# Kernel optimization log

Measured on AMD Instinct MI355X. Metric: run time of the kernel, lower is better.

## Reference

```python
import jax, jax.numpy as jnp
import numpy as np

N_E = 8192
E_DIM = 256
BETA = 0.25


def setup_inputs() -> dict:
    key = jax.random.key(0)
    k1, k2 = jax.random.split(key)
    z = jax.random.normal(k1, (16, E_DIM, 32, 32), dtype=jnp.float32)
    # matches torch init: uniform(-1/n_e, 1/n_e)
    emb_w = jax.random.uniform(k2, (N_E, E_DIM), dtype=jnp.float32,
                               minval=-1.0 / N_E, maxval=1.0 / N_E)
    return {"z": z, "emb_w": emb_w}


def reference(z, emb_w):
    B, C, H, W = z.shape
    zt = jnp.transpose(z, (0, 2, 3, 1))          # b h w c
    zf = zt.reshape(-1, C)                        # [N, e_dim]
    # d[n, k] = ||zf_n||^2 + ||e_k||^2 - 2 zf_n . e_k
    d = (jnp.sum(zf * zf, axis=1, keepdims=True)
         + jnp.sum(emb_w * emb_w, axis=1)
         - 2.0 * jnp.einsum('bd,nd->bn', zf, emb_w))
    idx = jnp.argmin(d, axis=1)                   # [N]
    z_q = emb_w[idx].reshape(zt.shape)            # b h w c
    sg = jax.lax.stop_gradient
    # legacy=True loss
    loss = jnp.mean((sg(z_q) - zt) ** 2) + BETA * jnp.mean((z_q - sg(zt)) ** 2)
    # straight-through estimator
    z_q_st = zt + sg(z_q - zt)
    z_q_out = jnp.transpose(z_q_st, (0, 3, 1, 2))  # b c h w
    return z_q_out, loss, idx.reshape(B, H, W)
```

## Files before the change

kernel.cpp:

```cpp
#include <hip/hip_runtime.h>
#include <math.h>

typedef unsigned int uint;
typedef unsigned short ushort;
typedef unsigned long long u64;
typedef __attribute__((ext_vector_type(8))) short short8;
typedef __attribute__((ext_vector_type(4))) float f32x4;

#define WS_ZT   0ull
#define WS_ZPK  16777216ull
#define WS_EPK  25165824ull
#define WS_SUMZ 29360128ull
#define WS_GMAX 29425664ull
#define WS_BEST 62980096ull
#define WS_LOSS 63111168ull

#define DOT_MARGIN 1.5e-4f

__device__ __forceinline__ ushort f2bf(float f) {
  uint b = __float_as_uint(f);
  b += 0x7fffu + ((b >> 16) & 1u);
  return (ushort)(b >> 16);
}
__device__ __forceinline__ uint ford(float f) {
  uint b = __float_as_uint(f);
  return (b & 0x80000000u) ? ~b : (b | 0x80000000u);
}
__device__ __forceinline__ void gload_lds16(const void* g, void* l) {
  __builtin_amdgcn_global_load_lds(
      (const __attribute__((address_space(1))) unsigned int*)g,
      (__attribute__((address_space(3))) unsigned int*)l, 16, 0, 0);
}

__global__ __launch_bounds__(256) void prep_z(const float* __restrict__ z,
                                              float* __restrict__ zt,
                                              ushort* __restrict__ zpk) {
  __shared__ float tile[64][65];
  const int bid = blockIdx.x;
  const int kt = bid & 3, hwt = (bid >> 2) & 15, b = bid >> 6;
  const int t = threadIdx.x, lane = t & 63, grp = t >> 6;
  const float* src = z + b * 262144 + (kt * 64) * 1024 + hwt * 64;
  for (int kk = grp; kk < 64; kk += 4)
    tile[kk][lane] = src[kk * 1024 + lane];
  __syncthreads();
  for (int rr = grp; rr < 64; rr += 4) {
    const int n = b * 1024 + hwt * 64 + rr;
    zt[n * 256 + kt * 64 + lane] = tile[lane][rr];
  }
  for (int u = t; u < 512; u += 256) {
    const int n_loc = u & 63, kg = u >> 6;
    const int n = b * 1024 + hwt * 64 + n_loc;
    const int k0 = kt * 64 + kg * 8;
    short8 s;
#pragma unroll
    for (int j = 0; j < 8; ++j) s[j] = (short)f2bf(tile[kg * 8 + j][n_loc]);
    *(short8*)(zpk + (size_t)(n >> 4) * 4096 + (k0 >> 5) * 512 +
               ((k0 >> 3) & 3) * 128 + (n & 15) * 8) = s;
  }
}

__global__ __launch_bounds__(256) void prep_e(const float* __restrict__ emb,
                                              ushort* __restrict__ epk) {
  const int u = blockIdx.x * 256 + threadIdx.x;
  const int c = u >> 5, k0 = (u & 31) * 8;
  const float4 v0 = *(const float4*)(emb + c * 256 + k0);
  const float4 v1 = *(const float4*)(emb + c * 256 + k0 + 4);
  short8 s;
  s[0] = (short)f2bf(v0.x); s[1] = (short)f2bf(v0.y);
  s[2] = (short)f2bf(v0.z); s[3] = (short)f2bf(v0.w);
  s[4] = (short)f2bf(v1.x); s[5] = (short)f2bf(v1.y);
  s[6] = (short)f2bf(v1.z); s[7] = (short)f2bf(v1.w);
  *(short8*)(epk + (size_t)(c >> 4) * 4096 + (k0 >> 5) * 512 +
             ((k0 >> 3) & 3) * 128 + (c & 15) * 8) = s;
}

__global__ __launch_bounds__(256) void zsum_kernel(const float* __restrict__ z,
                                                   float* __restrict__ sumz) {
  const int n = (blockIdx.x << 8) + threadIdx.x;
  const int b = n >> 10, hw = n & 1023;
  const float* zb = z + b * 262144 + hw;
  float s = 0.f;
#pragma unroll 8
  for (int c = 0; c < 256; ++c) { const float v = zb[c << 10]; s += v * v; }
  sumz[n] = s;
}

__global__ __launch_bounds__(256) void gemm_screen(const ushort* __restrict__ zpk,
                                                   const ushort* __restrict__ epk,
                                                   uint* __restrict__ gmax) {
  __shared__ ushort Cs[16384];
  const int t = threadIdx.x;
  const int w = t >> 6, lane = t & 63;
  const int bid = blockIdx.x;
  const int x = bid & 7, y = bid >> 3;
  const int colb = (y & 15) * 8 + x;
  const int rowg = y >> 4;
  const int n0 = rowg << 10;
  const int m16 = lane & 15, q = lane >> 4;
  const int cix = x * 64 + (y & 15) * 4 + q;

#pragma unroll
  for (int f2 = 0; f2 < 8; ++f2) {
    const int f = w * 8 + f2;
    gload_lds16(epk + (size_t)colb * 16384 + f * 512 + lane * 8, (char*)Cs + f * 1024);
  }

  short8 z0[4], z1[4], z2[4];
  const ushort* zs0 = zpk + ((size_t)(n0 >> 4) + w * 4) * 4096 + lane * 8;
#pragma unroll
  for (int jr = 0; jr < 4; ++jr) z0[jr] = *(const short8*)(zs0 + jr * 4096);
#pragma unroll
  for (int jr = 0; jr < 4; ++jr) z1[jr] = *(const short8*)(zs0 + jr * 4096 + 512);
  __syncthreads();

  for (int strip = 0; strip < 4; ++strip) {
    const int rbase = n0 + strip * 256 + w * 64;
    const ushort* zb = zpk + (size_t)(rbase >> 4) * 4096 + lane * 8;
    const ushort* zbn = (strip < 3) ? (zb + 16 * 4096) : zb;
    f32x4 acc[4][4];
#pragma unroll
    for (int i = 0; i < 4; ++i)
#pragma unroll
      for (int j = 0; j < 4; ++j) acc[i][j] = {0.f, 0.f, 0.f, 0.f};

#pragma unroll
    for (int s32 = 0; s32 < 8; ++s32) {
      const ushort* pf = (s32 < 6) ? (zb + (s32 + 2) * 512) : (zbn + (s32 - 6) * 512);
#pragma unroll
      for (int jr = 0; jr < 4; ++jr) z2[jr] = *(const short8*)(pf + jr * 4096);
      short8 cv[4];
#pragma unroll
      for (int ic = 0; ic < 4; ++ic)
        cv[ic] = *(const short8*)&Cs[(size_t)(ic * 8 + s32) * 512 + lane * 8];
#pragma unroll
      for (int ic = 0; ic < 4; ++ic)
#pragma unroll
        for (int jr = 0; jr < 4; ++jr)
          acc[ic][jr] = __builtin_amdgcn_mfma_f32_16x16x32_bf16(cv[ic], z0[jr],
                                                                acc[ic][jr], 0, 0, 0);
#pragma unroll
      for (int jr = 0; jr < 4; ++jr) { z0[jr] = z1[jr]; z1[jr] = z2[jr]; }
    }

#pragma unroll
    for (int jr = 0; jr < 4; ++jr) {
      uint pk[4];
#pragma unroll
      for (int ic = 0; ic < 4; ++ic) {
        float m = fmaxf(fmaxf(acc[ic][jr][0], acc[ic][jr][1]),
                        fmaxf(acc[ic][jr][2], acc[ic][jr][3]));
        m = fmaxf(m, __shfl_xor(m, 16, 64));
        const float o = __shfl_xor(m, 32, 64);
        const float glo = (q & 2) ? o : m;
        const float ghi = (q & 2) ? m : o;
        pk[ic] = (uint)f2bf(glo) | ((uint)f2bf(ghi) << 16);
      }
      const uint sv = (q == 0) ? pk[0] : (q == 1) ? pk[1] : (q == 2) ? pk[2] : pk[3];
      __builtin_nontemporal_store(sv,
          &gmax[(size_t)(rbase + jr * 16 + m16) * 512 + cix]);
    }
  }
}

__global__ __launch_bounds__(256) void select_rescore(const uint* __restrict__ gmax,
                                                      const float* __restrict__ zt,
                                                      const float* __restrict__ emb,
                                                      const float* __restrict__ sumz,
                                                      u64* __restrict__ best) {
  const int t = threadIdx.x, w = t >> 6, lane = t & 63;
  const int n = (blockIdx.x << 2) + w;
  __shared__ float zrow[4][256];
  __shared__ ushort hits[4][128];
  ((float4*)zrow[w])[lane] = ((const float4*)(zt + (size_t)n * 256))[lane];
  const uint4 r0 = ((const uint4*)(gmax + (size_t)n * 512))[lane];
  const uint4 r1 = ((const uint4*)(gmax + (size_t)n * 512))[lane + 64];
  const uint uv[8] = {r0.x, r0.y, r0.z, r0.w, r1.x, r1.y, r1.z, r1.w};
  float m = -INFINITY;
#pragma unroll
  for (int j = 0; j < 8; ++j) {
    m = fmaxf(m, __uint_as_float(uv[j] << 16));
    m = fmaxf(m, __uint_as_float(uv[j] & 0xffff0000u));
  }
#pragma unroll
  for (int off = 1; off < 64; off <<= 1) m = fmaxf(m, __shfl_xor(m, off, 64));
  const float thr = m - DOT_MARGIN;
  const u64 below = (1ull << lane) - 1ull;
  int base = 0;
#pragma unroll
  for (int j = 0; j < 8; ++j) {
    const int ui = (j < 4) ? lane * 4 + j : 256 + lane * 4 + (j - 4);
    {
      const bool hit = __uint_as_float(uv[j] << 16) >= thr;
      const u64 msk = __ballot(hit);
      if (hit) {
        const int p = base + (int)__popcll(msk & below);
        if (p < 128) hits[w][p] = (ushort)(ui * 2);
      }
      base += (int)__popcll(msk);
    }
    {
      const bool hit = __uint_as_float(uv[j] & 0xffff0000u) >= thr;
      const u64 msk = __ballot(hit);
      if (hit) {
        const int p = base + (int)__popcll(msk & below);
        if (p < 128) hits[w][p] = (ushort)(ui * 2 + 1);
      }
      base += (int)__popcll(msk);
    }
  }
  __threadfence_block();
  int K = base > 128 ? 128 : base;
  const float sz = sumz[n];
  u64 bk = ~0ull;
  for (int id = lane; id < K * 8; id += 64) {
    const int gid = hits[w][id >> 3];
    const int ci = gid >> 1, h = gid & 1;
    const int c = ((ci >> 2) & 15) * 512 + (ci >> 6) * 64 + (ci & 3) * 16 +
                  h * 8 + (id & 7);
    const float4* ea = (const float4*)(emb + c * 256);
    const float4* za = (const float4*)zrow[w];
    float sdot = 0.f, se = 0.f;
#pragma unroll 8
    for (int k = 0; k < 64; ++k) {
      const float4 a = za[k], e = ea[k];
      sdot = fmaf(a.x, e.x, sdot); sdot = fmaf(a.y, e.y, sdot);
      sdot = fmaf(a.z, e.z, sdot); sdot = fmaf(a.w, e.w, sdot);
      se = fmaf(e.x, e.x, se); se = fmaf(e.y, e.y, se);
      se = fmaf(e.z, e.z, se); se = fmaf(e.w, e.w, se);
    }
    const float d = (sz + se) - 2.f * sdot;
    const u64 key = ((u64)ford(d) << 32) | (uint)c;
    if (key < bk) bk = key;
  }
#pragma unroll
  for (int off = 1; off < 64; off <<= 1) {
    const u64 o = (((u64)(uint)__shfl_xor((int)(bk >> 32), off, 64)) << 32) |
                  (uint)__shfl_xor((int)(bk & 0xffffffffu), off, 64);
    if (o < bk) bk = o;
  }
  if (lane == 0) best[n] = bk;
}

__global__ __launch_bounds__(256) void gather_kernel(const float* __restrict__ z,
                                                     const float* __restrict__ emb,
                                                     const u64* __restrict__ best,
                                                     float* __restrict__ out,
                                                     double* __restrict__ loss_acc,
                                                     uint* __restrict__ done) {
  const int t = threadIdx.x;
  const int n0 = blockIdx.x << 6;
  const int n = n0 + (t & 63);
  const int idx = (int)(best[n] & 0xffffffffull);
  const int b_i = n >> 10, hw = n & 1023;
  const int c0 = t >> 6;
  const float* zb = z + b_i * 262144 + hw;
  float* ob = out + b_i * 262144 + hw;
  const float* eb = emb + idx * 256;
  float lsum = 0.f;
#pragma unroll 4
  for (int c = c0; c < 256; c += 4) {
    const float ev = eb[c];
    const float zv = zb[c << 10];
    ob[c << 10] = ev;
    const float d = ev - zv;
    lsum += d * d;
  }
  if (c0 == 0) out[4194305 + n] = (float)idx;
#pragma unroll
  for (int off = 32; off; off >>= 1) lsum += __shfl_down(lsum, off, 64);
  __shared__ double wsum[4];
  if ((t & 63) == 0) wsum[t >> 6] = (double)lsum;
  __syncthreads();
  if (t == 0) {
    atomicAdd(loss_acc, wsum[0] + wsum[1] + wsum[2] + wsum[3]);
    __threadfence();
    if (atomicAdd(done, 1u) == 255u) {
      __threadfence();
      out[4194304] = (float)(1.25 * (*(volatile double*)loss_acc) / 4194304.0);
    }
  }
}

extern "C" void kernel_launch(void* const* d_in, const int* in_sizes, int n_in,
                              void* d_out, int out_size, void* d_ws, size_t ws_size,
                              hipStream_t stream) {
  const float* z = (const float*)d_in[0];
  const float* emb = (const float*)d_in[1];
  float* out = (float*)d_out;
  char* ws = (char*)d_ws;
  float* zt = (float*)(ws + WS_ZT);
  ushort* zpk = (ushort*)(ws + WS_ZPK);
  ushort* epk = (ushort*)(ws + WS_EPK);
  float* sumz = (float*)(ws + WS_SUMZ);
  uint* gmax = (uint*)(ws + WS_GMAX);
  u64* best = (u64*)(ws + WS_BEST);
  double* loss_acc = (double*)(ws + WS_LOSS);
  uint* done = (uint*)(ws + WS_LOSS + 8);

  hipMemsetAsync(ws + WS_LOSS, 0, 16, stream);
  prep_z<<<1024, 256, 0, stream>>>(z, zt, zpk);
  prep_e<<<1024, 256, 0, stream>>>(emb, epk);
  zsum_kernel<<<64, 256, 0, stream>>>(z, sumz);
  gemm_screen<<<2048, 256, 0, stream>>>(zpk, epk, gmax);
  select_rescore<<<4096, 256, 0, stream>>>(gmax, zt, emb, sumz, best);
  gather_kernel<<<256, 256, 0, stream>>>(z, emb, best, out, loss_acc, done);
}
```

Before: 259.9 us.

## Merge prep kernels into one launch, deepen z prefetch, use plain gmax stores

Combines the three preprocessing kernels (z transpose/pack, embedding pack, z norm sums) into a single launch dispatched by block index. This removes two launches and their gaps. The GEMM screen kernel now prefetches z fragments three steps ahead instead of two, with a clamped continuous index across strips, to hide more global load latency at the cost of extra registers. The nontemporal store of gmax becomes a regular store, so the data can stay in cache for the following select kernel.

```diff
diff --git a/kernel.cpp b/kernel.cpp
--- a/kernel.cpp
+++ b/kernel.cpp
@@ -32,57 +32,58 @@
       (__attribute__((address_space(3))) unsigned int*)l, 16, 0, 0);
 }
 
-__global__ __launch_bounds__(256) void prep_z(const float* __restrict__ z,
-                                              float* __restrict__ zt,
-                                              ushort* __restrict__ zpk) {
+__global__ __launch_bounds__(256) void prep_all(const float* __restrict__ z,
+                                                const float* __restrict__ emb,
+                                                float* __restrict__ zt,
+                                                ushort* __restrict__ zpk,
+                                                ushort* __restrict__ epk,
+                                                float* __restrict__ sumz) {
   __shared__ float tile[64][65];
-  const int bid = blockIdx.x;
-  const int kt = bid & 3, hwt = (bid >> 2) & 15, b = bid >> 6;
-  const int t = threadIdx.x, lane = t & 63, grp = t >> 6;
-  const float* src = z + b * 262144 + (kt * 64) * 1024 + hwt * 64;
-  for (int kk = grp; kk < 64; kk += 4)
-    tile[kk][lane] = src[kk * 1024 + lane];
-  __syncthreads();
-  for (int rr = grp; rr < 64; rr += 4) {
-    const int n = b * 1024 + hwt * 64 + rr;
-    zt[n * 256 + kt * 64 + lane] = tile[lane][rr];
-  }
-  for (int u = t; u < 512; u += 256) {
-    const int n_loc = u & 63, kg = u >> 6;
-    const int n = b * 1024 + hwt * 64 + n_loc;
-    const int k0 = kt * 64 + kg * 8;
+  const int bidg = blockIdx.x;
+  const int t = threadIdx.x;
+  if (bidg < 1024) {
+    const int bid = bidg;
+    const int kt = bid & 3, hwt = (bid >> 2) & 15, b = bid >> 6;
+    const int lane = t & 63, grp = t >> 6;
+    const float* src = z + b * 262144 + (kt * 64) * 1024 + hwt * 64;
+    for (int kk = grp; kk < 64; kk += 4)
+      tile[kk][lane] = src[kk * 1024 + lane];
+    __syncthreads();
+    for (int rr = grp; rr < 64; rr += 4) {
+      const int n = b * 1024 + hwt * 64 + rr;
+      zt[n * 256 + kt * 64 + lane] = tile[lane][rr];
+    }
+    for (int u = t; u < 512; u += 256) {
+      const int n_loc = u & 63, kg = u >> 6;
+      const int n = b * 1024 + hwt * 64 + n_loc;
+      const int k0 = kt * 64 + kg * 8;
+      short8 s;
+#pragma unroll
+      for (int j = 0; j < 8; ++j) s[j] = (short)f2bf(tile[kg * 8 + j][n_loc]);
+      *(short8*)(zpk + (size_t)(n >> 4) * 4096 + (k0 >> 5) * 512 +
+                 ((k0 >> 3) & 3) * 128 + (n & 15) * 8) = s;
+    }
+  } else if (bidg < 2048) {
+    const int u = (bidg - 1024) * 256 + t;
+    const int c = u >> 5, k0 = (u & 31) * 8;
+    const float4 v0 = *(const float4*)(emb + c * 256 + k0);
+    const float4 v1 = *(const float4*)(emb + c * 256 + k0 + 4);
     short8 s;
-#pragma unroll
-    for (int j = 0; j < 8; ++j) s[j] = (short)f2bf(tile[kg * 8 + j][n_loc]);
-    *(short8*)(zpk + (size_t)(n >> 4) * 4096 + (k0 >> 5) * 512 +
-               ((k0 >> 3) & 3) * 128 + (n & 15) * 8) = s;
-  }
-}
-
-__global__ __launch_bounds__(256) void prep_e(const float* __restrict__ emb,
-                                              ushort* __restrict__ epk) {
-  const int u = blockIdx.x * 256 + threadIdx.x;
-  const int c = u >> 5, k0 = (u & 31) * 8;
-  const float4 v0 = *(const float4*)(emb + c * 256 + k0);
-  const float4 v1 = *(const float4*)(emb + c * 256 + k0 + 4);
-  short8 s;
-  s[0] = (short)f2bf(v0.x); s[1] = (short)f2bf(v0.y);
-  s[2] = (short)f2bf(v0.z); s[3] = (short)f2bf(v0.w);
-  s[4] = (short)f2bf(v1.x); s[5] = (short)f2bf(v1.y);
-  s[6] = (short)f2bf(v1.z); s[7] = (short)f2bf(v1.w);
-  *(short8*)(epk + (size_t)(c >> 4) * 4096 + (k0 >> 5) * 512 +
-             ((k0 >> 3) & 3) * 128 + (c & 15) * 8) = s;
-}
-
-__global__ __launch_bounds__(256) void zsum_kernel(const float* __restrict__ z,
-                                                   float* __restrict__ sumz) {
-  const int n = (blockIdx.x << 8) + threadIdx.x;
-  const int b = n >> 10, hw = n & 1023;
-  const float* zb = z + b * 262144 + hw;
-  float s = 0.f;
+    s[0] = (short)f2bf(v0.x); s[1] = (short)f2bf(v0.y);
+    s[2] = (short)f2bf(v0.z); s[3] = (short)f2bf(v0.w);
+    s[4] = (short)f2bf(v1.x); s[5] = (short)f2bf(v1.y);
+    s[6] = (short)f2bf(v1.z); s[7] = (short)f2bf(v1.w);
+    *(short8*)(epk + (size_t)(c >> 4) * 4096 + (k0 >> 5) * 512 +
+               ((k0 >> 3) & 3) * 128 + (c & 15) * 8) = s;
+  } else {
+    const int n = ((bidg - 2048) << 8) + t;
+    const int b = n >> 10, hw = n & 1023;
+    const float* zb = z + b * 262144 + hw;
+    float s = 0.f;
 #pragma unroll 8
-  for (int c = 0; c < 256; ++c) { const float v = zb[c << 10]; s += v * v; }
-  sumz[n] = s;
+    for (int c = 0; c < 256; ++c) { const float v = zb[c << 10]; s += v * v; }
+    sumz[n] = s;
+  }
 }
 
 __global__ __launch_bounds__(256) void gemm_screen(const ushort* __restrict__ zpk,
@@ -105,18 +106,19 @@
     gload_lds16(epk + (size_t)colb * 16384 + f * 512 + lane * 8, (char*)Cs + f * 1024);
   }
 
-  short8 z0[4], z1[4], z2[4];
-  const ushort* zs0 = zpk + ((size_t)(n0 >> 4) + w * 4) * 4096 + lane * 8;
-#pragma unroll
-  for (int jr = 0; jr < 4; ++jr) z0[jr] = *(const short8*)(zs0 + jr * 4096);
-#pragma unroll
-  for (int jr = 0; jr < 4; ++jr) z1[jr] = *(const short8*)(zs0 + jr * 4096 + 512);
+  const ushort* zw = zpk + ((size_t)(n0 >> 4) + w * 4) * 4096 + lane * 8;
+
+  short8 z0[4], z1[4], z2[4], z3[4];
+#pragma unroll
+  for (int jr = 0; jr < 4; ++jr) z0[jr] = *(const short8*)(zw + jr * 4096);
+#pragma unroll
+  for (int jr = 0; jr < 4; ++jr) z1[jr] = *(const short8*)(zw + jr * 4096 + 512);
+#pragma unroll
+  for (int jr = 0; jr < 4; ++jr) z2[jr] = *(const short8*)(zw + jr * 4096 + 1024);
   __syncthreads();
 
   for (int strip = 0; strip < 4; ++strip) {
     const int rbase = n0 + strip * 256 + w * 64;
-    const ushort* zb = zpk + (size_t)(rbase >> 4) * 4096 + lane * 8;
-    const ushort* zbn = (strip < 3) ? (zb + 16 * 4096) : zb;
     f32x4 acc[4][4];
 #pragma unroll
     for (int i = 0; i < 4; ++i)
@@ -125,9 +127,11 @@
 
 #pragma unroll
     for (int s32 = 0; s32 < 8; ++s32) {
-      const ushort* pf = (s32 < 6) ? (zb + (s32 + 2) * 512) : (zbn + (s32 - 6) * 512);
-#pragma unroll
-      for (int jr = 0; jr < 4; ++jr) z2[jr] = *(const short8*)(pf + jr * 4096);
+      const int v = strip * 8 + s32 + 3;
+      const int vv = v > 31 ? 31 : v;
+      const ushort* pf = zw + ((size_t)(vv >> 3) * 16) * 4096 + (vv & 7) * 512;
+#pragma unroll
+      for (int jr = 0; jr < 4; ++jr) z3[jr] = *(const short8*)(pf + jr * 4096);
       short8 cv[4];
 #pragma unroll
       for (int ic = 0; ic < 4; ++ic)
@@ -139,7 +143,9 @@
           acc[ic][jr] = __builtin_amdgcn_mfma_f32_16x16x32_bf16(cv[ic], z0[jr],
                                                                 acc[ic][jr], 0, 0, 0);
 #pragma unroll
-      for (int jr = 0; jr < 4; ++jr) { z0[jr] = z1[jr]; z1[jr] = z2[jr]; }
+      for (int jr = 0; jr < 4; ++jr) {
+        z0[jr] = z1[jr]; z1[jr] = z2[jr]; z2[jr] = z3[jr];
+      }
     }
 
 #pragma unroll
@@ -156,8 +162,7 @@
         pk[ic] = (uint)f2bf(glo) | ((uint)f2bf(ghi) << 16);
       }
       const uint sv = (q == 0) ? pk[0] : (q == 1) ? pk[1] : (q == 2) ? pk[2] : pk[3];
-      __builtin_nontemporal_store(sv,
-          &gmax[(size_t)(rbase + jr * 16 + m16) * 512 + cix]);
+      gmax[(size_t)(rbase + jr * 16 + m16) * 512 + cix] = sv;
     }
   }
 }
@@ -298,9 +303,7 @@
   uint* done = (uint*)(ws + WS_LOSS + 8);
 
   hipMemsetAsync(ws + WS_LOSS, 0, 16, stream);
-  prep_z<<<1024, 256, 0, stream>>>(z, zt, zpk);
-  prep_e<<<1024, 256, 0, stream>>>(emb, epk);
-  zsum_kernel<<<64, 256, 0, stream>>>(z, sumz);
+  prep_all<<<2112, 256, 0, stream>>>(z, emb, zt, zpk, epk, sumz);
   gemm_screen<<<2048, 256, 0, stream>>>(zpk, epk, gmax);
   select_rescore<<<4096, 256, 0, stream>>>(gmax, zt, emb, sumz, best);
   gather_kernel<<<256, 256, 0, stream>>>(z, emb, best, out, loss_acc, done);
```

Result: faster. 249.5 us (-4.0%).
